# Optimization experiments

Measured on AMD Instinct MI355X. Metric: run time of the kernel, lower is better.

Reference implementation:

```python
import jax, jax.numpy as jnp
import numpy as np

N_NODES = 50000
N_EDGES = 1000000
IN_FEATS = 128
OUT_FEATS = 16
NUM_HEADS = 4
ALPHA = 0.2  # LeakyReLU negative slope


def setup_inputs() -> dict:
    key = jax.random.key(0)
    k1, k2, k3, k4, k5 = jax.random.split(key, 5)
    edge_index = jax.random.randint(k1, (2, N_EDGES), 0, N_NODES, dtype=jnp.int64)
    h = jax.random.normal(k2, (N_NODES, IN_FEATS), dtype=jnp.float32)
    # xavier_uniform with gain=1.414 approximated by scaled normals (values irrelevant to math)
    W = jax.random.normal(k3, (IN_FEATS, OUT_FEATS * NUM_HEADS), dtype=jnp.float32) * 0.1
    a_src = jax.random.normal(k4, (1, NUM_HEADS, OUT_FEATS), dtype=jnp.float32) * 0.1
    a_dst = jax.random.normal(k5, (1, NUM_HEADS, OUT_FEATS), dtype=jnp.float32) * 0.1
    return {"edge_index": edge_index, "h": h, "W": W, "a_src": a_src, "a_dst": a_dst}


def reference(edge_index, h, W, a_src, a_dst):
    N = h.shape[0]
    Wh = (h @ W).reshape(N, NUM_HEADS, OUT_FEATS)          # [N, H, F]
    src, dst = edge_index[0], edge_index[1]
    Wh_src = Wh[src]                                        # [E, H, F] gather
    Wh_dst = Wh[dst]                                        # [E, H, F] gather
    e = (Wh_src * a_src).sum(-1) + (Wh_dst * a_dst).sum(-1)  # [E, H]
    e = jnp.where(e > 0, e, ALPHA * e)                       # LeakyReLU
    attention = jax.nn.softmax(e, axis=0)                    # softmax over ALL edges per head (as in source)
    # dropout omitted (eval mode / p effectively 0 for reference)
    msgs = attention[:, :, None] * Wh_src                    # [E, H, F]
    h_prime = jax.ops.segment_sum(msgs, dst, num_segments=N)  # scatter-add per dst
    h_prime = jax.nn.relu(h_prime)
    return h_prime.reshape(N, NUM_HEADS * OUT_FEATS)
```

## Files before the change

kernel.cpp:

```cpp
#include <hip/hip_runtime.h>
#include <hip/hip_bf16.h>

#define IN_F 128
#define OUT_F 16
#define N_HEADS 4
#define OUT_C 64
#define ALPHA 0.2f
#define EPB 4096
#define TILE 64

typedef __attribute__((ext_vector_type(8))) short bf16x8;
typedef __attribute__((ext_vector_type(4))) float f32x4;

__device__ __forceinline__ unsigned int enc_f(float f) {
  unsigned int u = __float_as_uint(f);
  return (u & 0x80000000u) ? ~u : (u | 0x80000000u);
}
__device__ __forceinline__ float dec_f(unsigned int u) {
  unsigned int b = (u & 0x80000000u) ? (u & 0x7FFFFFFFu) : ~u;
  return __uint_as_float(b);
}

__device__ __forceinline__ ushort f2bf(float f) {
  union { __hip_bfloat16 b; ushort u; } cv;
  cv.b = __float2bfloat16(f);
  return cv.u;
}
__device__ __forceinline__ float bf2f(ushort u) {
  return __uint_as_float(((unsigned int)u) << 16);
}

__global__ __launch_bounds__(1024) void k_init(unsigned int* gmax_s, unsigned int* gmax_d,
                                               float* gsum, int* btot, int nbkt) {
  int t = threadIdx.x;
  if (t < N_HEADS) {
    gmax_s[t] = enc_f(-3.0e38f);
    gmax_d[t] = enc_f(-3.0e38f);
    gsum[t] = 0.f;
  }
  for (int i = t; i < nbkt; i += 1024) btot[i] = 0;
}

__global__ __launch_bounds__(256) void k_pack(const float* __restrict__ W,
                                              uint4* __restrict__ Wp) {
  int lane = threadIdx.x & 63;
  int ks = threadIdx.x >> 6;
  int cl = lane & 15, kg = lane >> 4;
#pragma unroll
  for (int ct = 0; ct < 4; ++ct) {
    int c = ct * 16 + cl;
    int k0 = ks * 32 + kg * 8;
    union { ushort u[8]; uint4 q; } P;
#pragma unroll
    for (int j = 0; j < 8; ++j) P.u[j] = f2bf(W[(k0 + j) * OUT_C + c]);
    Wp[(ks * 4 + ct) * 64 + lane] = P.q;
  }
}

__global__ __launch_bounds__(256) void k_mm(
    const float* __restrict__ h, const uint4* __restrict__ Wp,
    const float* __restrict__ a_src, const float* __restrict__ a_dst,
    ushort* __restrict__ Whb, float4* __restrict__ ssrc4, float4* __restrict__ sdst4,
    unsigned int* __restrict__ gmax_s, unsigned int* __restrict__ gmax_d,
    int n_nodes)
{
  const int wid = threadIdx.x >> 6, lane = threadIdx.x & 63;
  const int r0 = blockIdx.x * 64 + wid * 16;
  const int arow = r0 + (lane & 15);
  const int rclamp = arow < n_nodes ? arow : n_nodes - 1;
  const float* hrow = h + (size_t)rclamp * IN_F + (lane >> 4) * 8;

  f32x4 acc[4];
#pragma unroll
  for (int ct = 0; ct < 4; ++ct) acc[ct] = (f32x4){0.f, 0.f, 0.f, 0.f};

#pragma unroll
  for (int ks = 0; ks < 4; ++ks) {
    float4 a0 = *(const float4*)(hrow + ks * 32);
    float4 a1 = *(const float4*)(hrow + ks * 32 + 4);
    union { ushort u[8]; bf16x8 v; } A;
    A.u[0] = f2bf(a0.x); A.u[1] = f2bf(a0.y); A.u[2] = f2bf(a0.z); A.u[3] = f2bf(a0.w);
    A.u[4] = f2bf(a1.x); A.u[5] = f2bf(a1.y); A.u[6] = f2bf(a1.z); A.u[7] = f2bf(a1.w);
#pragma unroll
    for (int ct = 0; ct < 4; ++ct) {
      union { uint4 q; bf16x8 v; } B;
      B.q = Wp[(ks * 4 + ct) * 64 + lane];
      acc[ct] = __builtin_amdgcn_mfma_f32_16x16x32_bf16(A.v, B.v, acc[ct], 0, 0, 0);
    }
  }

  const int cl = lane & 15, g = lane >> 4;
  float as_[4], ad_[4];
#pragma unroll
  for (int ct = 0; ct < 4; ++ct) { as_[ct] = a_src[ct * 16 + cl]; ad_[ct] = a_dst[ct * 16 + cl]; }

  float ms[4], md[4];
#pragma unroll
  for (int ct = 0; ct < 4; ++ct) { ms[ct] = -3.0e38f; md[ct] = -3.0e38f; }

#pragma unroll
  for (int j = 0; j < 4; ++j) {
    int r = r0 + g * 4 + j;
    bool rv = r < n_nodes;
    float ps[4], pd[4];
#pragma unroll
    for (int ct = 0; ct < 4; ++ct) {
      float v = acc[ct][j];
      if (rv) Whb[(size_t)r * OUT_C + ct * 16 + cl] = f2bf(v);
      ps[ct] = v * as_[ct];
      pd[ct] = v * ad_[ct];
    }
#pragma unroll
    for (int o = 1; o < 16; o <<= 1) {
#pragma unroll
      for (int ct = 0; ct < 4; ++ct) {
        ps[ct] += __shfl_xor(ps[ct], o);
        pd[ct] += __shfl_xor(pd[ct], o);
      }
    }
    if (rv && cl == 0) {
      ssrc4[r] = make_float4(ps[0], ps[1], ps[2], ps[3]);
      sdst4[r] = make_float4(pd[0], pd[1], pd[2], pd[3]);
    }
    if (rv) {
#pragma unroll
      for (int ct = 0; ct < 4; ++ct) {
        ms[ct] = fmaxf(ms[ct], ps[ct]);
        md[ct] = fmaxf(md[ct], pd[ct]);
      }
    }
  }
#pragma unroll
  for (int o = 16; o < 64; o <<= 1) {
#pragma unroll
    for (int ct = 0; ct < 4; ++ct) {
      ms[ct] = fmaxf(ms[ct], __shfl_xor(ms[ct], o));
      md[ct] = fmaxf(md[ct], __shfl_xor(md[ct], o));
    }
  }
  __shared__ float wmS[4][4], wmD[4][4];
  if (lane == 0) {
#pragma unroll
    for (int ct = 0; ct < 4; ++ct) { wmS[wid][ct] = ms[ct]; wmD[wid][ct] = md[ct]; }
  }
  __syncthreads();
  if (threadIdx.x < N_HEADS) {
    int t = threadIdx.x;
    float vs = fmaxf(fmaxf(wmS[0][t], wmS[1][t]), fmaxf(wmS[2][t], wmS[3][t]));
    float vd = fmaxf(fmaxf(wmD[0][t], wmD[1][t]), fmaxf(wmD[2][t], wmD[3][t]));
    atomicMax(gmax_s + t, enc_f(vs));
    atomicMax(gmax_d + t, enc_f(vd));
  }
}

__global__ __launch_bounds__(256) void k_part(
    const int* __restrict__ ei, int2* __restrict__ pairs,
    int* __restrict__ boff, int* __restrict__ btot, int n_edges, int nbkt)
{
  const int base = blockIdx.x * EPB;
  const int n = min(EPB, n_edges - base);
  const int t = threadIdx.x;
  __shared__ int lh[1024];
  __shared__ int lw[1024];
  __shared__ int ts[256];
  __shared__ int2 buf[EPB];

  for (int i = t; i < 1024; i += 256) lh[i] = 0;
  __syncthreads();

  int4 sv[4], dv[4];
#pragma unroll
  for (int k = 0; k < 4; ++k) {
    int q4 = k * 256 + t;
    int e0 = q4 * 4;
    if (e0 + 3 < n) {
      sv[k] = ((const int4*)(ei + base))[q4];
      dv[k] = ((const int4*)(ei + n_edges + base))[q4];
    } else {
      int s0 = 0, s1 = 0, s2 = 0, s3 = 0, d0 = -1, d1 = -1, d2 = -1, d3 = -1;
      if (e0 + 0 < n) { s0 = ei[base + e0];     d0 = ei[n_edges + base + e0]; }
      if (e0 + 1 < n) { s1 = ei[base + e0 + 1]; d1 = ei[n_edges + base + e0 + 1]; }
      if (e0 + 2 < n) { s2 = ei[base + e0 + 2]; d2 = ei[n_edges + base + e0 + 2]; }
      if (e0 + 3 < n) { s3 = ei[base + e0 + 3]; d3 = ei[n_edges + base + e0 + 3]; }
      sv[k] = make_int4(s0, s1, s2, s3);
      dv[k] = make_int4(d0, d1, d2, d3);
    }
    int dd[4] = {dv[k].x, dv[k].y, dv[k].z, dv[k].w};
#pragma unroll
    for (int q = 0; q < 4; ++q)
      if (dd[q] >= 0) atomicAdd(&lh[dd[q] >> 6], 1);
  }
  __syncthreads();

  {
    int b0 = t * 4;
    int c0 = lh[b0], c1 = lh[b0 + 1], c2 = lh[b0 + 2], c3 = lh[b0 + 3];
    int my = c0 + c1 + c2 + c3;
    ts[t] = my;
    __syncthreads();
#pragma unroll
    for (int off = 1; off < 256; off <<= 1) {
      int v = (t >= off) ? ts[t - off] : 0;
      __syncthreads();
      ts[t] += v;
      __syncthreads();
    }
    int ex = ts[t] - my;
    lh[b0] = ex; ex += c0;
    lh[b0 + 1] = ex; ex += c1;
    lh[b0 + 2] = ex; ex += c2;
    lh[b0 + 3] = ex;
  }
  __syncthreads();
  for (int i = t; i < 1024; i += 256) lw[i] = lh[i];
  __syncthreads();

#pragma unroll
  for (int k = 0; k < 4; ++k) {
    int ss[4] = {sv[k].x, sv[k].y, sv[k].z, sv[k].w};
    int dd[4] = {dv[k].x, dv[k].y, dv[k].z, dv[k].w};
#pragma unroll
    for (int q = 0; q < 4; ++q) {
      if (dd[q] >= 0) {
        int pos = atomicAdd(&lw[dd[q] >> 6], 1);
        buf[pos] = make_int2(ss[q], dd[q]);
      }
    }
  }
  __syncthreads();

  for (int i = t; i < n; i += 256) pairs[(size_t)base + i] = buf[i];
  for (int i = t; i <= nbkt; i += 256)
    boff[(size_t)blockIdx.x * (nbkt + 1) + i] = (i < nbkt) ? lh[i] : n;
  for (int i = t; i < nbkt; i += 256) {
    int c = lw[i] - lh[i];
    if (c) atomicAdd(&btot[i], c);
  }
}

__global__ __launch_bounds__(1024) void k_gscan(
    const int* __restrict__ btot, int* __restrict__ gbase, int nbkt)
{
  __shared__ int sd[1024];
  int t = threadIdx.x;
  int c = (t < nbkt) ? btot[t] : 0;
  sd[t] = c;
  __syncthreads();
#pragma unroll
  for (int off = 1; off < 1024; off <<= 1) {
    int v = (t >= off) ? sd[t - off] : 0;
    __syncthreads();
    sd[t] += v;
    __syncthreads();
  }
  if (t < nbkt) gbase[t] = sd[t] - c;
}

__global__ __launch_bounds__(256) void k_sortb(
    const int2* __restrict__ pairs, const int* __restrict__ boff,
    const int* __restrict__ gbase, const float4* __restrict__ ssrc4,
    const float4* __restrict__ sdst4, const unsigned int* __restrict__ gmax_s,
    const unsigned int* __restrict__ gmax_d, float* __restrict__ gsum,
    int* __restrict__ sorted_src, int* __restrict__ offs,
    int npb, int nbkt, int n_edges, int n_nodes)
{
  const int b = blockIdx.x;
  const int t = threadIdx.x;
  __shared__ int ts[256];
  __shared__ int hist[65];
  __shared__ int hcur[64];
  __shared__ int totsh;
  __shared__ int2 buf1[4096];
  __shared__ int2 buf2[4096];

  int cnt = 0, bo = 0;
  if (t < npb) {
    const int* bp = boff + (size_t)t * (nbkt + 1) + b;
    bo = bp[0];
    cnt = bp[1] - bo;
  }
  ts[t] = cnt;
  __syncthreads();
#pragma unroll
  for (int off = 1; off < 256; off <<= 1) {
    int v = (t >= off) ? ts[t - off] : 0;
    __syncthreads();
    ts[t] += v;
    __syncthreads();
  }
  int base = ts[t] - cnt;
  if (t == 255) totsh = ts[255];
  for (int i = t; i < 65; i += 256) hist[i] = 0;
  __syncthreads();
  const int total = min(totsh, 4096);

  if (cnt > 0 && base < 4096) {
    const int2* rp = pairs + (size_t)t * EPB + bo;
    int lim = min(cnt, 4096 - base);
    for (int j = 0; j < lim; ++j) buf1[base + j] = rp[j];
  }
  __syncthreads();

  for (int i = t; i < total; i += 256) atomicAdd(&hist[buf1[i].y & 63], 1);
  __syncthreads();
  if (t == 0) {
    int run = 0;
#pragma unroll
    for (int i = 0; i < 64; ++i) { int c = hist[i]; hist[i] = run; run += c; }
    hist[64] = run;
  }
  __syncthreads();
  for (int i = t; i < 64; i += 256) hcur[i] = hist[i];
  __syncthreads();
  for (int i = t; i < total; i += 256) {
    int2 p = buf1[i];
    int pos = atomicAdd(&hcur[p.y & 63], 1);
    buf2[pos] = p;
  }
  __syncthreads();

  const int gb = gbase[b];
  float M[4];
#pragma unroll
  for (int c = 0; c < 4; ++c) {
    float m = dec_f(gmax_s[c]) + dec_f(gmax_d[c]);
    M[c] = m > 0.f ? m : ALPHA * m;
  }
  float acc[4] = {0.f, 0.f, 0.f, 0.f};
  for (int i = t; i < total; i += 256) {
    int2 p = buf2[i];
    sorted_src[gb + i] = p.x;
    float4 a = ssrc4[p.x];
    float4 bb = sdst4[p.y];
    float e0 = a.x + bb.x; e0 = e0 > 0.f ? e0 : ALPHA * e0;
    float e1 = a.y + bb.y; e1 = e1 > 0.f ? e1 : ALPHA * e1;
    float e2 = a.z + bb.z; e2 = e2 > 0.f ? e2 : ALPHA * e2;
    float e3 = a.w + bb.w; e3 = e3 > 0.f ? e3 : ALPHA * e3;
    acc[0] += __expf(e0 - M[0]); acc[1] += __expf(e1 - M[1]);
    acc[2] += __expf(e2 - M[2]); acc[3] += __expf(e3 - M[3]);
  }

  if (t <= 64) {
    int d = b * TILE + t;
    if (d <= n_nodes) offs[d] = gb + hist[t];
  }

  __shared__ float red[4][4];
  int lane = t & 63, wv = t >> 6;
#pragma unroll
  for (int c = 0; c < 4; ++c)
#pragma unroll
    for (int o = 32; o; o >>= 1) acc[c] += __shfl_down(acc[c], o);
  if (lane == 0) { red[wv][0] = acc[0]; red[wv][1] = acc[1]; red[wv][2] = acc[2]; red[wv][3] = acc[3]; }
  __syncthreads();
  if (t < 4) {
    float v = red[0][t] + red[1][t] + red[2][t] + red[3][t];
    atomicAdd(gsum + t, v);
  }
}

__global__ __launch_bounds__(256) void k_agg(
    const int* __restrict__ offs, const int* __restrict__ sorted_src,
    const float* __restrict__ ssrc, const float4* __restrict__ sdst4,
    const ushort* __restrict__ Whb, const unsigned int* __restrict__ gmax_s,
    const unsigned int* __restrict__ gmax_d, const float* __restrict__ gsum,
    float* __restrict__ out, int n_nodes)
{
  int d = blockIdx.x * 4 + (threadIdx.x >> 6);
  if (d >= n_nodes) return;
  const int lane = threadIdx.x & 63;
  const int g = lane >> 4;
  const int c4 = lane & 15;
  const int head = c4 >> 2;
  float m = dec_f(gmax_s[head]) + dec_f(gmax_d[head]);
  float M = m > 0.f ? m : ALPHA * m;
  float inv = 1.f / gsum[head];
  float4 sd4 = sdst4[d];
  float sdh = head == 0 ? sd4.x : head == 1 ? sd4.y : head == 2 ? sd4.z : sd4.w;

  int beg = offs[d], end = offs[d + 1];
  float a0 = 0.f, a1 = 0.f, a2 = 0.f, a3 = 0.f;
#pragma unroll 2
  for (int j = beg; j < end; j += 4) {
    int je = j + g;
    bool val = je < end;
    int s = sorted_src[val ? je : beg];
    float sc = ssrc[s * N_HEADS + head] + sdh;
    sc = sc > 0.f ? sc : ALPHA * sc;
    float w = __expf(sc - M);
    w = val ? w : 0.f;
    ushort4 v = *(const ushort4*)(Whb + (size_t)s * OUT_C + c4 * 4);
    a0 += w * bf2f(v.x);
    a1 += w * bf2f(v.y);
    a2 += w * bf2f(v.z);
    a3 += w * bf2f(v.w);
  }
  a0 += __shfl_xor(a0, 16); a1 += __shfl_xor(a1, 16);
  a2 += __shfl_xor(a2, 16); a3 += __shfl_xor(a3, 16);
  a0 += __shfl_xor(a0, 32); a1 += __shfl_xor(a1, 32);
  a2 += __shfl_xor(a2, 32); a3 += __shfl_xor(a3, 32);
  if (g == 0) {
    float4 o;
    o.x = fmaxf(a0 * inv, 0.f);
    o.y = fmaxf(a1 * inv, 0.f);
    o.z = fmaxf(a2 * inv, 0.f);
    o.w = fmaxf(a3 * inv, 0.f);
    ((float4*)(out + (size_t)d * OUT_C))[c4] = o;
  }
}

extern "C" void kernel_launch(void* const* d_in, const int* in_sizes, int n_in,
                              void* d_out, int out_size, void* d_ws, size_t ws_size,
                              hipStream_t stream) {
  const int*   ei    = (const int*)d_in[0];
  const float* h     = (const float*)d_in[1];
  const float* W     = (const float*)d_in[2];
  const float* a_src = (const float*)d_in[3];
  const float* a_dst = (const float*)d_in[4];
  float* out = (float*)d_out;

  const int n_edges = in_sizes[0] / 2;
  const int n_nodes = in_sizes[1] / IN_F;
  const int npb     = (n_edges + EPB - 1) / EPB;
  const int nbkt    = (n_nodes + TILE - 1) / TILE;

  char* ws = (char*)d_ws;
  size_t off = 0;
  auto alloc = [&](size_t bytes) { void* p = ws + off; off = (off + bytes + 15) & ~(size_t)15; return p; };
  ushort* Whb         = (ushort*)alloc((size_t)n_nodes * OUT_C * 2);
  float* ssrc         = (float*)alloc((size_t)n_nodes * N_HEADS * 4);
  float* sdst         = (float*)alloc((size_t)n_nodes * N_HEADS * 4);
  unsigned int* gmax_s= (unsigned int*)alloc(N_HEADS * 4);
  unsigned int* gmax_d= (unsigned int*)alloc(N_HEADS * 4);
  float* gsum         = (float*)alloc(N_HEADS * 4);
  int* btot           = (int*)alloc((size_t)nbkt * 4);
  int* gbase          = (int*)alloc((size_t)nbkt * 4);
  int* offs           = (int*)alloc(((size_t)n_nodes + 1) * 4);
  int* sorted_src     = (int*)alloc((size_t)n_edges * 4);
  int2* pairs         = (int2*)alloc((size_t)npb * EPB * 8);
  int* boff           = (int*)alloc((size_t)npb * (nbkt + 1) * 4);
  uint4* Wp           = (uint4*)alloc(16 * 64 * 16);

  k_init<<<1, 1024, 0, stream>>>(gmax_s, gmax_d, gsum, btot, nbkt);
  k_pack<<<1, 256, 0, stream>>>(W, Wp);
  k_mm<<<(n_nodes + 63) / 64, 256, 0, stream>>>(h, Wp, a_src, a_dst, Whb,
      (float4*)ssrc, (float4*)sdst, gmax_s, gmax_d, n_nodes);
  k_part<<<npb, 256, 0, stream>>>(ei, pairs, boff, btot, n_edges, nbkt);
  k_gscan<<<1, 1024, 0, stream>>>(btot, gbase, nbkt);
  k_sortb<<<nbkt, 256, 0, stream>>>(pairs, boff, gbase, (const float4*)ssrc,
      (const float4*)sdst, gmax_s, gmax_d, gsum, sorted_src, offs,
      npb, nbkt, n_edges, n_nodes);
  k_agg<<<(n_nodes + 3) / 4, 256, 0, stream>>>(offs, sorted_src, ssrc,
      (const float4*)sdst, Whb, gmax_s, gmax_d, gsum, out, n_nodes);
}
```

Before: 114.7 us.

## Merge init/pack, fuse matmul with edge partition, drop global scan kernel

Merges the init and W-pack kernels into one launch, and runs the edge-partition blocks and the matmul blocks inside a single kernel so they execute concurrently. The separate bucket-offset scan kernel is removed; each sort block now sums the preceding bucket totals itself, which adds redundant reads of btot per block. The second shared buffer in the sort kernel is dropped by writing sorted_src directly at the scattered position while computing the softmax partial sums. The aggregation loop is unrolled manually to handle two edges per group per iteration, raising memory-level parallelism. The fused kernel now reserves the partition kernel's large shared-memory footprint for the matmul blocks as well, which may lower their occupancy.

```diff
diff --git a/kernel.cpp b/kernel.cpp
--- a/kernel.cpp
+++ b/kernel.cpp
@@ -30,21 +30,20 @@
   return __uint_as_float(((unsigned int)u) << 16);
 }
 
-__global__ __launch_bounds__(1024) void k_init(unsigned int* gmax_s, unsigned int* gmax_d,
-                                               float* gsum, int* btot, int nbkt) {
+__global__ __launch_bounds__(256) void k_initpack(
+    const float* __restrict__ W, uint4* __restrict__ Wp,
+    unsigned int* gmax_s, unsigned int* gmax_d, float* gsum,
+    int* btot, int nbkt)
+{
   int t = threadIdx.x;
   if (t < N_HEADS) {
     gmax_s[t] = enc_f(-3.0e38f);
     gmax_d[t] = enc_f(-3.0e38f);
     gsum[t] = 0.f;
   }
-  for (int i = t; i < nbkt; i += 1024) btot[i] = 0;
-}
-
-__global__ __launch_bounds__(256) void k_pack(const float* __restrict__ W,
-                                              uint4* __restrict__ Wp) {
-  int lane = threadIdx.x & 63;
-  int ks = threadIdx.x >> 6;
+  for (int i = t; i < nbkt; i += 256) btot[i] = 0;
+  int lane = t & 63;
+  int ks = t >> 6;
   int cl = lane & 15, kg = lane >> 4;
 #pragma unroll
   for (int ct = 0; ct < 4; ++ct) {
@@ -57,15 +56,104 @@
   }
 }
 
-__global__ __launch_bounds__(256) void k_mm(
+__global__ __launch_bounds__(256) void k_mmpart(
     const float* __restrict__ h, const uint4* __restrict__ Wp,
     const float* __restrict__ a_src, const float* __restrict__ a_dst,
     ushort* __restrict__ Whb, float4* __restrict__ ssrc4, float4* __restrict__ sdst4,
     unsigned int* __restrict__ gmax_s, unsigned int* __restrict__ gmax_d,
-    int n_nodes)
+    const int* __restrict__ ei, int2* __restrict__ pairs,
+    int* __restrict__ boff, int* __restrict__ btot,
+    int n_nodes, int n_edges, int nbkt, int npb)
 {
-  const int wid = threadIdx.x >> 6, lane = threadIdx.x & 63;
-  const int r0 = blockIdx.x * 64 + wid * 16;
+  __shared__ int lh[1024];
+  __shared__ int lw[1024];
+  __shared__ int tsx[256];
+  __shared__ int2 pbuf[EPB];
+  __shared__ float wmS[4][4], wmD[4][4];
+
+  const int t = threadIdx.x;
+
+  if (blockIdx.x < (unsigned)npb) {
+    const int base = blockIdx.x * EPB;
+    const int n = min(EPB, n_edges - base);
+
+    for (int i = t; i < 1024; i += 256) lh[i] = 0;
+    __syncthreads();
+
+    int4 sv[4], dv[4];
+#pragma unroll
+    for (int k = 0; k < 4; ++k) {
+      int q4 = k * 256 + t;
+      int e0 = q4 * 4;
+      if (e0 + 3 < n) {
+        sv[k] = ((const int4*)(ei + base))[q4];
+        dv[k] = ((const int4*)(ei + n_edges + base))[q4];
+      } else {
+        int s0 = 0, s1 = 0, s2 = 0, s3 = 0, d0 = -1, d1 = -1, d2 = -1, d3 = -1;
+        if (e0 + 0 < n) { s0 = ei[base + e0];     d0 = ei[n_edges + base + e0]; }
+        if (e0 + 1 < n) { s1 = ei[base + e0 + 1]; d1 = ei[n_edges + base + e0 + 1]; }
+        if (e0 + 2 < n) { s2 = ei[base + e0 + 2]; d2 = ei[n_edges + base + e0 + 2]; }
+        if (e0 + 3 < n) { s3 = ei[base + e0 + 3]; d3 = ei[n_edges + base + e0 + 3]; }
+        sv[k] = make_int4(s0, s1, s2, s3);
+        dv[k] = make_int4(d0, d1, d2, d3);
+      }
+      int dd[4] = {dv[k].x, dv[k].y, dv[k].z, dv[k].w};
+#pragma unroll
+      for (int q = 0; q < 4; ++q)
+        if (dd[q] >= 0) atomicAdd(&lh[dd[q] >> 6], 1);
+    }
+    __syncthreads();
+
+    {
+      int b0 = t * 4;
+      int c0 = lh[b0], c1 = lh[b0 + 1], c2 = lh[b0 + 2], c3 = lh[b0 + 3];
+      int my = c0 + c1 + c2 + c3;
+      tsx[t] = my;
+      __syncthreads();
+#pragma unroll
+      for (int off = 1; off < 256; off <<= 1) {
+        int v = (t >= off) ? tsx[t - off] : 0;
+        __syncthreads();
+        tsx[t] += v;
+        __syncthreads();
+      }
+      int ex = tsx[t] - my;
+      lh[b0] = ex; ex += c0;
+      lh[b0 + 1] = ex; ex += c1;
+      lh[b0 + 2] = ex; ex += c2;
+      lh[b0 + 3] = ex;
+    }
+    __syncthreads();
+    for (int i = t; i < 1024; i += 256) lw[i] = lh[i];
+    __syncthreads();
+
+#pragma unroll
+    for (int k = 0; k < 4; ++k) {
+      int ss[4] = {sv[k].x, sv[k].y, sv[k].z, sv[k].w};
+      int dd[4] = {dv[k].x, dv[k].y, dv[k].z, dv[k].w};
+#pragma unroll
+      for (int q = 0; q < 4; ++q) {
+        if (dd[q] >= 0) {
+          int pos = atomicAdd(&lw[dd[q] >> 6], 1);
+          pbuf[pos] = make_int2(ss[q], dd[q]);
+        }
+      }
+    }
+    __syncthreads();
+
+    for (int i = t; i < n; i += 256) pairs[(size_t)base + i] = pbuf[i];
+    for (int i = t; i <= nbkt; i += 256)
+      boff[(size_t)blockIdx.x * (nbkt + 1) + i] = (i < nbkt) ? lh[i] : n;
+    for (int i = t; i < nbkt; i += 256) {
+      int c = lw[i] - lh[i];
+      if (c) atomicAdd(&btot[i], c);
+    }
+    return;
+  }
+
+  const int bid = blockIdx.x - npb;
+  const int wid = t >> 6, lane = t & 63;
+  const int r0 = bid * 64 + wid * 16;
   const int arow = r0 + (lane & 15);
   const int rclamp = arow < n_nodes ? arow : n_nodes - 1;
   const float* hrow = h + (size_t)rclamp * IN_F + (lane >> 4) * 8;
@@ -138,14 +226,12 @@
       md[ct] = fmaxf(md[ct], __shfl_xor(md[ct], o));
     }
   }
-  __shared__ float wmS[4][4], wmD[4][4];
   if (lane == 0) {
 #pragma unroll
     for (int ct = 0; ct < 4; ++ct) { wmS[wid][ct] = ms[ct]; wmD[wid][ct] = md[ct]; }
   }
   __syncthreads();
-  if (threadIdx.x < N_HEADS) {
-    int t = threadIdx.x;
+  if (t < N_HEADS) {
     float vs = fmaxf(fmaxf(wmS[0][t], wmS[1][t]), fmaxf(wmS[2][t], wmS[3][t]));
     float vd = fmaxf(fmaxf(wmD[0][t], wmD[1][t]), fmaxf(wmD[2][t], wmD[3][t]));
     atomicMax(gmax_s + t, enc_f(vs));
@@ -153,112 +239,9 @@
   }
 }
 
-__global__ __launch_bounds__(256) void k_part(
-    const int* __restrict__ ei, int2* __restrict__ pairs,
-    int* __restrict__ boff, int* __restrict__ btot, int n_edges, int nbkt)
-{
-  const int base = blockIdx.x * EPB;
-  const int n = min(EPB, n_edges - base);
-  const int t = threadIdx.x;
-  __shared__ int lh[1024];
-  __shared__ int lw[1024];
-  __shared__ int ts[256];
-  __shared__ int2 buf[EPB];
-
-  for (int i = t; i < 1024; i += 256) lh[i] = 0;
-  __syncthreads();
-
-  int4 sv[4], dv[4];
-#pragma unroll
-  for (int k = 0; k < 4; ++k) {
-    int q4 = k * 256 + t;
-    int e0 = q4 * 4;
-    if (e0 + 3 < n) {
-      sv[k] = ((const int4*)(ei + base))[q4];
-      dv[k] = ((const int4*)(ei + n_edges + base))[q4];
-    } else {
-      int s0 = 0, s1 = 0, s2 = 0, s3 = 0, d0 = -1, d1 = -1, d2 = -1, d3 = -1;
-      if (e0 + 0 < n) { s0 = ei[base + e0];     d0 = ei[n_edges + base + e0]; }
-      if (e0 + 1 < n) { s1 = ei[base + e0 + 1]; d1 = ei[n_edges + base + e0 + 1]; }
-      if (e0 + 2 < n) { s2 = ei[base + e0 + 2]; d2 = ei[n_edges + base + e0 + 2]; }
-      if (e0 + 3 < n) { s3 = ei[base + e0 + 3]; d3 = ei[n_edges + base + e0 + 3]; }
-      sv[k] = make_int4(s0, s1, s2, s3);
-      dv[k] = make_int4(d0, d1, d2, d3);
-    }
-    int dd[4] = {dv[k].x, dv[k].y, dv[k].z, dv[k].w};
-#pragma unroll
-    for (int q = 0; q < 4; ++q)
-      if (dd[q] >= 0) atomicAdd(&lh[dd[q] >> 6], 1);
-  }
-  __syncthreads();
-
-  {
-    int b0 = t * 4;
-    int c0 = lh[b0], c1 = lh[b0 + 1], c2 = lh[b0 + 2], c3 = lh[b0 + 3];
-    int my = c0 + c1 + c2 + c3;
-    ts[t] = my;
-    __syncthreads();
-#pragma unroll
-    for (int off = 1; off < 256; off <<= 1) {
-      int v = (t >= off) ? ts[t - off] : 0;
-      __syncthreads();
-      ts[t] += v;
-      __syncthreads();
-    }
-    int ex = ts[t] - my;
-    lh[b0] = ex; ex += c0;
-    lh[b0 + 1] = ex; ex += c1;
-    lh[b0 + 2] = ex; ex += c2;
-    lh[b0 + 3] = ex;
-  }
-  __syncthreads();
-  for (int i = t; i < 1024; i += 256) lw[i] = lh[i];
-  __syncthreads();
-
-#pragma unroll
-  for (int k = 0; k < 4; ++k) {
-    int ss[4] = {sv[k].x, sv[k].y, sv[k].z, sv[k].w};
-    int dd[4] = {dv[k].x, dv[k].y, dv[k].z, dv[k].w};
-#pragma unroll
-    for (int q = 0; q < 4; ++q) {
-      if (dd[q] >= 0) {
-        int pos = atomicAdd(&lw[dd[q] >> 6], 1);
-        buf[pos] = make_int2(ss[q], dd[q]);
-      }
-    }
-  }
-  __syncthreads();
-
-  for (int i = t; i < n; i += 256) pairs[(size_t)base + i] = buf[i];
-  for (int i = t; i <= nbkt; i += 256)
-    boff[(size_t)blockIdx.x * (nbkt + 1) + i] = (i < nbkt) ? lh[i] : n;
-  for (int i = t; i < nbkt; i += 256) {
-    int c = lw[i] - lh[i];
-    if (c) atomicAdd(&btot[i], c);
-  }
-}
-
-__global__ __launch_bounds__(1024) void k_gscan(
-    const int* __restrict__ btot, int* __restrict__ gbase, int nbkt)
-{
-  __shared__ int sd[1024];
-  int t = threadIdx.x;
-  int c = (t < nbkt) ? btot[t] : 0;
-  sd[t] = c;
-  __syncthreads();
-#pragma unroll
-  for (int off = 1; off < 1024; off <<= 1) {
-    int v = (t >= off) ? sd[t - off] : 0;
-    __syncthreads();
-    sd[t] += v;
-    __syncthreads();
-  }
-  if (t < nbkt) gbase[t] = sd[t] - c;
-}
-
 __global__ __launch_bounds__(256) void k_sortb(
     const int2* __restrict__ pairs, const int* __restrict__ boff,
-    const int* __restrict__ gbase, const float4* __restrict__ ssrc4,
+    const int* __restrict__ btot, const float4* __restrict__ ssrc4,
     const float4* __restrict__ sdst4, const unsigned int* __restrict__ gmax_s,
     const unsigned int* __restrict__ gmax_d, float* __restrict__ gsum,
     int* __restrict__ sorted_src, int* __restrict__ offs,
@@ -266,12 +249,22 @@
 {
   const int b = blockIdx.x;
   const int t = threadIdx.x;
+  const int lane = t & 63, wv = t >> 6;
   __shared__ int ts[256];
   __shared__ int hist[65];
   __shared__ int hcur[64];
-  __shared__ int totsh;
+  __shared__ int totsh, gbsh;
+  __shared__ int gred[4];
+  __shared__ float red[4][4];
   __shared__ int2 buf1[4096];
-  __shared__ int2 buf2[4096];
+
+  {
+    int partial = 0;
+    for (int i = t; i < b; i += 256) partial += btot[i];
+#pragma unroll
+    for (int o = 32; o; o >>= 1) partial += __shfl_down(partial, o);
+    if (lane == 0) gred[wv] = partial;
+  }
 
   int cnt = 0, bo = 0;
   if (t < npb) {
@@ -281,6 +274,7 @@
   }
   ts[t] = cnt;
   __syncthreads();
+  if (t == 0) gbsh = gred[0] + gred[1] + gred[2] + gred[3];
 #pragma unroll
   for (int off = 1; off < 256; off <<= 1) {
     int v = (t >= off) ? ts[t - off] : 0;
@@ -293,6 +287,7 @@
   for (int i = t; i < 65; i += 256) hist[i] = 0;
   __syncthreads();
   const int total = min(totsh, 4096);
+  const int gb = gbsh;
 
   if (cnt > 0 && base < 4096) {
     const int2* rp = pairs + (size_t)t * EPB + bo;
@@ -312,32 +307,31 @@
   __syncthreads();
   for (int i = t; i < 64; i += 256) hcur[i] = hist[i];
   __syncthreads();
+
+  float M0, M1, M2, M3;
+  {
+    float m0 = dec_f(gmax_s[0]) + dec_f(gmax_d[0]);
+    float m1 = dec_f(gmax_s[1]) + dec_f(gmax_d[1]);
+    float m2 = dec_f(gmax_s[2]) + dec_f(gmax_d[2]);
+    float m3 = dec_f(gmax_s[3]) + dec_f(gmax_d[3]);
+    M0 = m0 > 0.f ? m0 : ALPHA * m0;
+    M1 = m1 > 0.f ? m1 : ALPHA * m1;
+    M2 = m2 > 0.f ? m2 : ALPHA * m2;
+    M3 = m3 > 0.f ? m3 : ALPHA * m3;
+  }
+  float ac0 = 0.f, ac1 = 0.f, ac2 = 0.f, ac3 = 0.f;
   for (int i = t; i < total; i += 256) {
     int2 p = buf1[i];
     int pos = atomicAdd(&hcur[p.y & 63], 1);
-    buf2[pos] = p;
-  }
-  __syncthreads();
-
-  const int gb = gbase[b];
-  float M[4];
-#pragma unroll
-  for (int c = 0; c < 4; ++c) {
-    float m = dec_f(gmax_s[c]) + dec_f(gmax_d[c]);
-    M[c] = m > 0.f ? m : ALPHA * m;
-  }
-  float acc[4] = {0.f, 0.f, 0.f, 0.f};
-  for (int i = t; i < total; i += 256) {
-    int2 p = buf2[i];
-    sorted_src[gb + i] = p.x;
+    sorted_src[gb + pos] = p.x;
     float4 a = ssrc4[p.x];
     float4 bb = sdst4[p.y];
     float e0 = a.x + bb.x; e0 = e0 > 0.f ? e0 : ALPHA * e0;
     float e1 = a.y + bb.y; e1 = e1 > 0.f ? e1 : ALPHA * e1;
     float e2 = a.z + bb.z; e2 = e2 > 0.f ? e2 : ALPHA * e2;
     float e3 = a.w + bb.w; e3 = e3 > 0.f ? e3 : ALPHA * e3;
-    acc[0] += __expf(e0 - M[0]); acc[1] += __expf(e1 - M[1]);
-    acc[2] += __expf(e2 - M[2]); acc[3] += __expf(e3 - M[3]);
+    ac0 += __expf(e0 - M0); ac1 += __expf(e1 - M1);
+    ac2 += __expf(e2 - M2); ac3 += __expf(e3 - M3);
   }
 
   if (t <= 64) {
@@ -345,13 +339,12 @@
     if (d <= n_nodes) offs[d] = gb + hist[t];
   }
 
-  __shared__ float red[4][4];
-  int lane = t & 63, wv = t >> 6;
-#pragma unroll
-  for (int c = 0; c < 4; ++c)
-#pragma unroll
-    for (int o = 32; o; o >>= 1) acc[c] += __shfl_down(acc[c], o);
-  if (lane == 0) { red[wv][0] = acc[0]; red[wv][1] = acc[1]; red[wv][2] = acc[2]; red[wv][3] = acc[3]; }
+#pragma unroll
+  for (int o = 32; o; o >>= 1) {
+    ac0 += __shfl_down(ac0, o); ac1 += __shfl_down(ac1, o);
+    ac2 += __shfl_down(ac2, o); ac3 += __shfl_down(ac3, o);
+  }
+  if (lane == 0) { red[wv][0] = ac0; red[wv][1] = ac1; red[wv][2] = ac2; red[wv][3] = ac3; }
   __syncthreads();
   if (t < 4) {
     float v = red[0][t] + red[1][t] + red[2][t] + red[3][t];
@@ -380,20 +373,25 @@
 
   int beg = offs[d], end = offs[d + 1];
   float a0 = 0.f, a1 = 0.f, a2 = 0.f, a3 = 0.f;
-#pragma unroll 2
-  for (int j = beg; j < end; j += 4) {
-    int je = j + g;
-    bool val = je < end;
-    int s = sorted_src[val ? je : beg];
-    float sc = ssrc[s * N_HEADS + head] + sdh;
-    sc = sc > 0.f ? sc : ALPHA * sc;
-    float w = __expf(sc - M);
-    w = val ? w : 0.f;
-    ushort4 v = *(const ushort4*)(Whb + (size_t)s * OUT_C + c4 * 4);
-    a0 += w * bf2f(v.x);
-    a1 += w * bf2f(v.y);
-    a2 += w * bf2f(v.z);
-    a3 += w * bf2f(v.w);
+  for (int j = beg; j < end; j += 8) {
+    int je0 = j + g, je1 = j + 4 + g;
+    bool v0 = je0 < end, v1 = je1 < end;
+    int s0 = sorted_src[v0 ? je0 : beg];
+    int s1 = sorted_src[v1 ? je1 : beg];
+    float sc0 = ssrc[s0 * N_HEADS + head] + sdh;
+    float sc1 = ssrc[s1 * N_HEADS + head] + sdh;
+    sc0 = sc0 > 0.f ? sc0 : ALPHA * sc0;
+    sc1 = sc1 > 0.f ? sc1 : ALPHA * sc1;
+    float w0 = __expf(sc0 - M);
+    float w1 = __expf(sc1 - M);
+    w0 = v0 ? w0 : 0.f;
+    w1 = v1 ? w1 : 0.f;
+    ushort4 va = *(const ushort4*)(Whb + (size_t)s0 * OUT_C + c4 * 4);
+    ushort4 vb = *(const ushort4*)(Whb + (size_t)s1 * OUT_C + c4 * 4);
+    a0 += w0 * bf2f(va.x) + w1 * bf2f(vb.x);
+    a1 += w0 * bf2f(va.y) + w1 * bf2f(vb.y);
+    a2 += w0 * bf2f(va.z) + w1 * bf2f(vb.z);
+    a3 += w0 * bf2f(va.w) + w1 * bf2f(vb.w);
   }
   a0 += __shfl_xor(a0, 16); a1 += __shfl_xor(a1, 16);
   a2 += __shfl_xor(a2, 16); a3 += __shfl_xor(a3, 16);
@@ -423,6 +421,7 @@
   const int n_nodes = in_sizes[1] / IN_F;
   const int npb     = (n_edges + EPB - 1) / EPB;
   const int nbkt    = (n_nodes + TILE - 1) / TILE;
+  const int nmm     = (n_nodes + 63) / 64;
 
   char* ws = (char*)d_ws;
   size_t off = 0;
@@ -434,20 +433,17 @@
   unsigned int* gmax_d= (unsigned int*)alloc(N_HEADS * 4);
   float* gsum         = (float*)alloc(N_HEADS * 4);
   int* btot           = (int*)alloc((size_t)nbkt * 4);
-  int* gbase          = (int*)alloc((size_t)nbkt * 4);
   int* offs           = (int*)alloc(((size_t)n_nodes + 1) * 4);
   int* sorted_src     = (int*)alloc((size_t)n_edges * 4);
   int2* pairs         = (int2*)alloc((size_t)npb * EPB * 8);
   int* boff           = (int*)alloc((size_t)npb * (nbkt + 1) * 4);
   uint4* Wp           = (uint4*)alloc(16 * 64 * 16);
 
-  k_init<<<1, 1024, 0, stream>>>(gmax_s, gmax_d, gsum, btot, nbkt);
-  k_pack<<<1, 256, 0, stream>>>(W, Wp);
-  k_mm<<<(n_nodes + 63) / 64, 256, 0, stream>>>(h, Wp, a_src, a_dst, Whb,
-      (float4*)ssrc, (float4*)sdst, gmax_s, gmax_d, n_nodes);
-  k_part<<<npb, 256, 0, stream>>>(ei, pairs, boff, btot, n_edges, nbkt);
-  k_gscan<<<1, 1024, 0, stream>>>(btot, gbase, nbkt);
-  k_sortb<<<nbkt, 256, 0, stream>>>(pairs, boff, gbase, (const float4*)ssrc,
+  k_initpack<<<1, 256, 0, stream>>>(W, Wp, gmax_s, gmax_d, gsum, btot, nbkt);
+  k_mmpart<<<npb + nmm, 256, 0, stream>>>(h, Wp, a_src, a_dst, Whb,
+      (float4*)ssrc, (float4*)sdst, gmax_s, gmax_d,
+      ei, pairs, boff, btot, n_nodes, n_edges, nbkt, npb);
+  k_sortb<<<nbkt, 256, 0, stream>>>(pairs, boff, btot, (const float4*)ssrc,
       (const float4*)sdst, gmax_s, gmax_d, gsum, sorted_src, offs,
       npb, nbkt, n_edges, n_nodes);
   k_agg<<<(n_nodes + 3) / 4, 256, 0, stream>>>(offs, sorted_src, ssrc,
```

Measured after the change: 98.39 us, median of 2. -14.2%, faster.
